# Performance work log

Hardware: AMD Instinct MI355X
Metric: run time of the kernel (lower is better)

Reference implementation:

```python
import jax, jax.numpy as jnp
import numpy as np

IGNORE_LABEL = 7
BETA = 1.0 / 9.0  # smooth-L1 beta from fastrcnn_loss


def setup_inputs() -> dict:
    key = jax.random.key(0)
    k = jax.random.split(key, 12)
    N, C, K, HM, G = 1024, 8, 17, 56, 256
    class_logits = jax.random.normal(k[0], (N, C), dtype=jnp.float32)
    box_regression = jax.random.normal(k[1], (N, C * 4), dtype=jnp.float32)
    regression_targets = jax.random.normal(k[2], (N, 4), dtype=jnp.float32) * 0.2
    # valid xyxy proposals in a ~1000px tile, widths/heights in [8, 64]
    x1 = jax.random.uniform(k[3], (N,)) * 900.0
    y1 = jax.random.uniform(k[4], (N,)) * 900.0
    w = 8.0 + jax.random.uniform(k[5], (N,)) * 56.0
    h = 8.0 + jax.random.uniform(k[6], (N,)) * 56.0
    proposals = jnp.stack([x1, y1, x1 + w, y1 + h], axis=1)
    # ground-truth keypoints: (x, y, visibility)
    kp_xy = jax.random.uniform(k[7], (G, K, 2)) * 1000.0
    kp_vis = (jax.random.uniform(k[8], (G, K, 1)) > 0.3).astype(jnp.float32)
    gt_keypoints = jnp.concatenate([kp_xy, kp_vis], axis=-1)
    keypoint_logits = jax.random.normal(k[9], (N, K, HM, HM), dtype=jnp.float32)
    labels = jax.random.randint(k[10], (N,), 0, C)
    keypoint_matched_idxs = jax.random.randint(k[11], (N,), 0, G)
    return {
        "class_logits": class_logits,
        "box_regression": box_regression,
        "regression_targets": regression_targets,
        "proposals": proposals,
        "gt_keypoints": gt_keypoints,
        "keypoint_logits": keypoint_logits,
        "labels": labels,
        "keypoint_matched_idxs": keypoint_matched_idxs,
    }


def _masked_ce(logits, targets, mask):
    # cross entropy averaged over masked entries (== F.cross_entropy on the subset)
    logp = jax.nn.log_softmax(logits, axis=-1)
    nll = -jnp.take_along_axis(logp, targets[:, None], axis=1)[:, 0]
    cnt = jnp.maximum(jnp.sum(mask.astype(logits.dtype)), 1.0)
    return jnp.sum(jnp.where(mask, nll, 0.0)) / cnt


def reference(class_logits, box_regression, regression_targets, proposals,
              gt_keypoints, keypoint_logits, labels, keypoint_matched_idxs):
    N, C = class_logits.shape
    # ---- fastrcnn_loss ----
    clkeep = labels != IGNORE_LABEL
    classification_loss = _masked_ce(class_logits, labels, clkeep)

    pos = labels > 0  # sampled_pos_inds_subset
    br = box_regression.reshape(N, C, 4)
    sel = jnp.take_along_axis(br, labels[:, None, None], axis=1)[:, 0, :]  # [N,4]
    d = sel - regression_targets
    ad = jnp.abs(d)
    sl1 = jnp.where(ad < BETA, 0.5 * d * d / BETA, ad - 0.5 * BETA)  # smooth_l1, sum
    box_loss = jnp.sum(jnp.where(pos[:, None], sl1, 0.0)) / N

    # ---- keypointrcnn_loss (keypoints_to_heatmap + CE over H*W bins) ----
    Nk, K, H, W = keypoint_logits.shape  # H == W == discretization_size
    kp = gt_keypoints[keypoint_matched_idxs]  # [N,K,3]
    ox, oy = proposals[:, 0:1], proposals[:, 1:2]
    sx = H / (proposals[:, 2:3] - proposals[:, 0:1])
    sy = H / (proposals[:, 3:4] - proposals[:, 1:2])
    kx, ky, vis = kp[..., 0], kp[..., 1], kp[..., 2]
    x = jnp.floor((kx - ox) * sx).astype(jnp.int32)
    y = jnp.floor((ky - oy) * sy).astype(jnp.int32)
    x = jnp.where(kx == proposals[:, 2:3], H - 1, x)
    y = jnp.where(ky == proposals[:, 3:4], H - 1, y)
    valid = (x >= 0) & (y >= 0) & (x < H) & (y < H) & (vis > 0)
    lin = (y * H + x) * valid.astype(jnp.int32)  # invalid entries -> bin 0 (masked out)
    kp_logits = keypoint_logits.reshape(Nk * K, H * W)
    keypoint_loss = _masked_ce(kp_logits, lin.reshape(-1), valid.reshape(-1))

    return jnp.stack([classification_loss, box_loss, keypoint_loss])
```

## Files before the change

### kernel.cpp

```cpp
#include <hip/hip_runtime.h>
#include <math.h>

#define K_KP 17
#define HM 56
#define HW (HM * HM)
#define N_ROWS 1024
#define NK_ROWS (N_ROWS * K_KP)
#define KP_BLOCKS ((NK_ROWS + 3) / 4)
#define C_CLS 8
#define IGNORE_LABEL 7
#define BETA_C (1.0f / 9.0f)

#define WS_FLOATS 515

__global__ __launch_bounds__(256) void roiheads_fused(
    const float* __restrict__ class_logits,
    const float* __restrict__ box_regression,
    const float* __restrict__ regression_targets,
    const float* __restrict__ proposals,
    const float* __restrict__ gt_keypoints,
    const float* __restrict__ keypoint_logits,
    const int*   __restrict__ labels,
    const int*   __restrict__ kmi,
    float* __restrict__ ws)
{
    const int bid = blockIdx.x;
    const int tid = threadIdx.x;

    if (bid < KP_BLOCKS) {
        const int lane = tid & 63;
        const int wid  = tid >> 6;
        const int r = bid * 4 + wid;
        if (r >= NK_ROWS) return;

        const int n = r / K_KP;
        const int k = r - n * K_KP;

        const int g = kmi[n];
        const float* kp = gt_keypoints + ((size_t)g * K_KP + k) * 3;
        const float kx  = kp[0];
        const float ky  = kp[1];
        const float vis = kp[2];
        const float px1 = proposals[n * 4 + 0];
        const float py1 = proposals[n * 4 + 1];
        const float px2 = proposals[n * 4 + 2];
        const float py2 = proposals[n * 4 + 3];
        const float sx = (float)HM / (px2 - px1);
        const float sy = (float)HM / (py2 - py1);
        int xi = (int)floorf((kx - px1) * sx);
        int yi = (int)floorf((ky - py1) * sy);
        if (kx == px2) xi = HM - 1;
        if (ky == py2) yi = HM - 1;
        const bool valid = (xi >= 0) & (yi >= 0) & (xi < HM) & (yi < HM) & (vis > 0.0f);
        if (!valid) return;

        const int lin = yi * HM + xi;
        const float4* rowp = (const float4*)(keypoint_logits + (size_t)r * HW);

        float m = -INFINITY, s = 0.0f;
        #pragma unroll
        for (int it = 0; it < 13; ++it) {
            const int idx = it * 64 + lane;
            if (idx < HW / 4) {
                const float4 v = rowp[idx];
                float vals[4] = {v.x, v.y, v.z, v.w};
                #pragma unroll
                for (int j = 0; j < 4; ++j) {
                    const float x = vals[j];
                    if (x > m) { s = s * expf(m - x) + 1.0f; m = x; }
                    else       { s += expf(x - m); }
                }
            }
        }
        #pragma unroll
        for (int off = 32; off > 0; off >>= 1) {
            const float om = __shfl_down(m, off, 64);
            const float os = __shfl_down(s, off, 64);
            const float nm = fmaxf(m, om);
            s = s * expf(m - nm) + os * expf(om - nm);
            m = nm;
        }
        if (lane == 0) {
            const float xt = keypoint_logits[(size_t)r * HW + lin];
            const float nll = m + logf(s) - xt;
            atomicAdd(&ws[r & 255], nll);
            atomicAdd(&ws[256 + (r & 255)], 1.0f);
        }
    } else {
        const int n = (bid - KP_BLOCKS) * 256 + tid;
        const int label = labels[n];

        const float* cl = class_logits + (size_t)n * C_CLS;
        float m = cl[0];
        #pragma unroll
        for (int j = 1; j < C_CLS; ++j) m = fmaxf(m, cl[j]);
        float s = 0.0f;
        #pragma unroll
        for (int j = 0; j < C_CLS; ++j) s += expf(cl[j] - m);
        const float nll = m + logf(s) - cl[label];
        const float keep = (label != IGNORE_LABEL) ? 1.0f : 0.0f;
        float cls_part = keep * nll;
        float keep_part = keep;

        float box_part = 0.0f;
        if (label > 0) {
            #pragma unroll
            for (int j = 0; j < 4; ++j) {
                const float d = box_regression[(size_t)n * 32 + label * 4 + j]
                              - regression_targets[(size_t)n * 4 + j];
                const float ad = fabsf(d);
                box_part += (ad < BETA_C) ? 0.5f * d * d / BETA_C : ad - 0.5f * BETA_C;
            }
        }

        #pragma unroll
        for (int off = 32; off > 0; off >>= 1) {
            cls_part  += __shfl_down(cls_part,  off, 64);
            keep_part += __shfl_down(keep_part, off, 64);
            box_part  += __shfl_down(box_part,  off, 64);
        }
        if ((tid & 63) == 0) {
            atomicAdd(&ws[512], cls_part);
            atomicAdd(&ws[513], keep_part);
            atomicAdd(&ws[514], box_part);
        }
    }
}

__global__ __launch_bounds__(256) void roiheads_finalize(
    const float* __restrict__ ws, float* __restrict__ out)
{
    __shared__ float sm_s[4];
    __shared__ float sm_c[4];
    const int tid = threadIdx.x;
    float ks = ws[tid];
    float kc = ws[256 + tid];
    #pragma unroll
    for (int off = 32; off > 0; off >>= 1) {
        ks += __shfl_down(ks, off, 64);
        kc += __shfl_down(kc, off, 64);
    }
    const int wid = tid >> 6;
    if ((tid & 63) == 0) { sm_s[wid] = ks; sm_c[wid] = kc; }
    __syncthreads();
    if (tid == 0) {
        const float S  = sm_s[0] + sm_s[1] + sm_s[2] + sm_s[3];
        const float Cn = sm_c[0] + sm_c[1] + sm_c[2] + sm_c[3];
        out[0] = ws[512] / fmaxf(ws[513], 1.0f);
        out[1] = ws[514] / (float)N_ROWS;
        out[2] = S / fmaxf(Cn, 1.0f);
    }
}

extern "C" void kernel_launch(void* const* d_in, const int* in_sizes, int n_in,
                              void* d_out, int out_size, void* d_ws, size_t ws_size,
                              hipStream_t stream) {
    const float* class_logits       = (const float*)d_in[0];
    const float* box_regression     = (const float*)d_in[1];
    const float* regression_targets = (const float*)d_in[2];
    const float* proposals          = (const float*)d_in[3];
    const float* gt_keypoints       = (const float*)d_in[4];
    const float* keypoint_logits    = (const float*)d_in[5];
    const int*   labels             = (const int*)d_in[6];
    const int*   kmi                = (const int*)d_in[7];
    float* ws  = (float*)d_ws;
    float* out = (float*)d_out;

    hipMemsetAsync(ws, 0, WS_FLOATS * sizeof(float), stream);

    const int total_blocks = KP_BLOCKS + (N_ROWS / 256);
    roiheads_fused<<<total_blocks, 256, 0, stream>>>(
        class_logits, box_regression, regression_targets, proposals,
        gt_keypoints, keypoint_logits, labels, kmi, ws);

    roiheads_finalize<<<1, 256, 0, stream>>>(ws, out);
}
```

Measured before the change: 272.5 us.

## Compact valid keypoint rows per block and replace global atomics with slot reduction

Each of 68 blocks now checks validity for 256 keypoint rows at once and appends the valid rows to a shared-memory queue. Its four waves then run the softmax cross-entropy only over the queued rows, which replaces thousands of small blocks that mostly exited early. Per-block partial sums go to fixed workspace slots, and the finalize kernel reduces them. This removes the memset and the global atomics. The tradeoff is less parallelism when many rows are valid, since each wave processes its rows one after another.

```diff
diff --git a/kernel.cpp b/kernel.cpp
--- a/kernel.cpp
+++ b/kernel.cpp
@@ -6,14 +6,14 @@
 #define HW (HM * HM)
 #define N_ROWS 1024
 #define NK_ROWS (N_ROWS * K_KP)
-#define KP_BLOCKS ((NK_ROWS + 3) / 4)
+#define KP_META_BLOCKS (NK_ROWS / 256)
+#define GRID (KP_META_BLOCKS + 1)
 #define C_CLS 8
 #define IGNORE_LABEL 7
 #define BETA_C (1.0f / 9.0f)
 
-#define WS_FLOATS 515
 
-__global__ __launch_bounds__(256) void roiheads_fused(
+__global__ __launch_bounds__(256) void roiheads_main(
     const float* __restrict__ class_logits,
     const float* __restrict__ box_regression,
     const float* __restrict__ regression_targets,
@@ -24,131 +24,154 @@
     const int*   __restrict__ kmi,
     float* __restrict__ ws)
 {
-    const int bid = blockIdx.x;
-    const int tid = threadIdx.x;
+    const int bid  = blockIdx.x;
+    const int tid  = threadIdx.x;
+    const int lane = tid & 63;
+    const int wid  = tid >> 6;
 
-    if (bid < KP_BLOCKS) {
-        const int lane = tid & 63;
-        const int wid  = tid >> 6;
-        const int r = bid * 4 + wid;
-        if (r >= NK_ROWS) return;
+    __shared__ int   q_r[256];
+    __shared__ int   q_lin[256];
+    __shared__ int   q_cnt;
+    __shared__ float w0[4], w1[4], w2[4];
 
+    float p0 = 0.0f, p1 = 0.0f, p2 = 0.0f, p3 = 0.0f, p4 = 0.0f;
+
+    if (bid < KP_META_BLOCKS) {
+        if (tid == 0) q_cnt = 0;
+        __syncthreads();
+
+        const int r = bid * 256 + tid;
         const int n = r / K_KP;
         const int k = r - n * K_KP;
-
         const int g = kmi[n];
         const float* kp = gt_keypoints + ((size_t)g * K_KP + k) * 3;
         const float kx  = kp[0];
         const float ky  = kp[1];
         const float vis = kp[2];
-        const float px1 = proposals[n * 4 + 0];
-        const float py1 = proposals[n * 4 + 1];
-        const float px2 = proposals[n * 4 + 2];
-        const float py2 = proposals[n * 4 + 3];
-        const float sx = (float)HM / (px2 - px1);
-        const float sy = (float)HM / (py2 - py1);
-        int xi = (int)floorf((kx - px1) * sx);
-        int yi = (int)floorf((ky - py1) * sy);
-        if (kx == px2) xi = HM - 1;
-        if (ky == py2) yi = HM - 1;
+        const float4 pr = ((const float4*)proposals)[n];
+        const float sx = (float)HM / (pr.z - pr.x);
+        const float sy = (float)HM / (pr.w - pr.y);
+        int xi = (int)floorf((kx - pr.x) * sx);
+        int yi = (int)floorf((ky - pr.y) * sy);
+        if (kx == pr.z) xi = HM - 1;
+        if (ky == pr.w) yi = HM - 1;
         const bool valid = (xi >= 0) & (yi >= 0) & (xi < HM) & (yi < HM) & (vis > 0.0f);
-        if (!valid) return;
+        if (valid) {
+            const int p = atomicAdd(&q_cnt, 1);
+            q_r[p]   = r;
+            q_lin[p] = yi * HM + xi;
+        }
+        __syncthreads();
+        const int cnt = q_cnt;
 
-        const int lin = yi * HM + xi;
-        const float4* rowp = (const float4*)(keypoint_logits + (size_t)r * HW);
-
-        float m = -INFINITY, s = 0.0f;
+        float my_s = 0.0f, my_c = 0.0f;
+        for (int i = wid; i < cnt; i += 4) {
+            const int rr = q_r[i];
+            const float* row = keypoint_logits + (size_t)rr * HW;
+            const float4* rp = (const float4*)row;
+            float m = -INFINITY, s = 0.0f;
+            #pragma unroll
+            for (int it = 0; it < 13; ++it) {
+                const int idx = it * 64 + lane;
+                if (idx < HW / 4) {
+                    const float4 v = rp[idx];
+                    float vals[4] = {v.x, v.y, v.z, v.w};
+                    #pragma unroll
+                    for (int j = 0; j < 4; ++j) {
+                        const float x = vals[j];
+                        if (x > m) { s = s * expf(m - x) + 1.0f; m = x; }
+                        else       { s += expf(x - m); }
+                    }
+                }
+            }
+            #pragma unroll
+            for (int off = 32; off > 0; off >>= 1) {
+                const float om = __shfl_down(m, off, 64);
+                const float os = __shfl_down(s, off, 64);
+                const float nm = fmaxf(m, om);
+                s = s * expf(m - nm) + os * expf(om - nm);
+                m = nm;
+            }
+            if (lane == 0) {
+                const float xt = row[q_lin[i]];
+                my_s += m + logf(s) - xt;
+                my_c += 1.0f;
+            }
+        }
+        if (lane == 0) { w0[wid] = my_s; w1[wid] = my_c; }
+        __syncthreads();
+        if (tid == 0) {
+            p0 = w0[0] + w0[1] + w0[2] + w0[3];
+            p1 = w1[0] + w1[1] + w1[2] + w1[3];
+        }
+    } else {
+        float cls_part = 0.0f, keep_part = 0.0f, box_part = 0.0f;
         #pragma unroll
-        for (int it = 0; it < 13; ++it) {
-            const int idx = it * 64 + lane;
-            if (idx < HW / 4) {
-                const float4 v = rowp[idx];
-                float vals[4] = {v.x, v.y, v.z, v.w};
+        for (int j = 0; j < 4; ++j) {
+            const int n = j * 256 + tid;
+            const int label = labels[n];
+            const float* cl = class_logits + (size_t)n * C_CLS;
+            float m = cl[0];
+            #pragma unroll
+            for (int c = 1; c < C_CLS; ++c) m = fmaxf(m, cl[c]);
+            float s = 0.0f;
+            #pragma unroll
+            for (int c = 0; c < C_CLS; ++c) s += expf(cl[c] - m);
+            const float nll  = m + logf(s) - cl[label];
+            const float keep = (label != IGNORE_LABEL) ? 1.0f : 0.0f;
+            cls_part  += keep * nll;
+            keep_part += keep;
+            if (label > 0) {
                 #pragma unroll
-                for (int j = 0; j < 4; ++j) {
-                    const float x = vals[j];
-                    if (x > m) { s = s * expf(m - x) + 1.0f; m = x; }
-                    else       { s += expf(x - m); }
+                for (int c = 0; c < 4; ++c) {
+                    const float d = box_regression[(size_t)n * 32 + label * 4 + c]
+                                  - regression_targets[(size_t)n * 4 + c];
+                    const float ad = fabsf(d);
+                    box_part += (ad < BETA_C) ? 0.5f * d * d / BETA_C : ad - 0.5f * BETA_C;
                 }
             }
         }
-        #pragma unroll
-        for (int off = 32; off > 0; off >>= 1) {
-            const float om = __shfl_down(m, off, 64);
-            const float os = __shfl_down(s, off, 64);
-            const float nm = fmaxf(m, om);
-            s = s * expf(m - nm) + os * expf(om - nm);
-            m = nm;
-        }
-        if (lane == 0) {
-            const float xt = keypoint_logits[(size_t)r * HW + lin];
-            const float nll = m + logf(s) - xt;
-            atomicAdd(&ws[r & 255], nll);
-            atomicAdd(&ws[256 + (r & 255)], 1.0f);
-        }
-    } else {
-        const int n = (bid - KP_BLOCKS) * 256 + tid;
-        const int label = labels[n];
-
-        const float* cl = class_logits + (size_t)n * C_CLS;
-        float m = cl[0];
-        #pragma unroll
-        for (int j = 1; j < C_CLS; ++j) m = fmaxf(m, cl[j]);
-        float s = 0.0f;
-        #pragma unroll
-        for (int j = 0; j < C_CLS; ++j) s += expf(cl[j] - m);
-        const float nll = m + logf(s) - cl[label];
-        const float keep = (label != IGNORE_LABEL) ? 1.0f : 0.0f;
-        float cls_part = keep * nll;
-        float keep_part = keep;
-
-        float box_part = 0.0f;
-        if (label > 0) {
-            #pragma unroll
-            for (int j = 0; j < 4; ++j) {
-                const float d = box_regression[(size_t)n * 32 + label * 4 + j]
-                              - regression_targets[(size_t)n * 4 + j];
-                const float ad = fabsf(d);
-                box_part += (ad < BETA_C) ? 0.5f * d * d / BETA_C : ad - 0.5f * BETA_C;
-            }
-        }
-
         #pragma unroll
         for (int off = 32; off > 0; off >>= 1) {
             cls_part  += __shfl_down(cls_part,  off, 64);
             keep_part += __shfl_down(keep_part, off, 64);
             box_part  += __shfl_down(box_part,  off, 64);
         }
-        if ((tid & 63) == 0) {
-            atomicAdd(&ws[512], cls_part);
-            atomicAdd(&ws[513], keep_part);
-            atomicAdd(&ws[514], box_part);
+        if (lane == 0) { w0[wid] = cls_part; w1[wid] = keep_part; w2[wid] = box_part; }
+        __syncthreads();
+        if (tid == 0) {
+            p2 = w0[0] + w0[1] + w0[2] + w0[3];
+            p3 = w1[0] + w1[1] + w1[2] + w1[3];
+            p4 = w2[0] + w2[1] + w2[2] + w2[3];
         }
+    }
+
+    if (tid == 0) {
+        float* slot = ws + (size_t)bid * 5;
+        slot[0] = p0; slot[1] = p1; slot[2] = p2; slot[3] = p3; slot[4] = p4;
     }
 }
 
-__global__ __launch_bounds__(256) void roiheads_finalize(
+__global__ __launch_bounds__(128) void roiheads_finalize(
     const float* __restrict__ ws, float* __restrict__ out)
 {
-    __shared__ float sm_s[4];
-    __shared__ float sm_c[4];
+    __shared__ float acc[5];
     const int tid = threadIdx.x;
-    float ks = ws[tid];
-    float kc = ws[256 + tid];
+    if (tid < 5) acc[tid] = 0.0f;
+    __syncthreads();
+    float v[5] = {0.0f, 0.0f, 0.0f, 0.0f, 0.0f};
+    if (tid < GRID) {
+        const float* slot = ws + (size_t)tid * 5;
+        #pragma unroll
+        for (int j = 0; j < 5; ++j) v[j] = slot[j];
+    }
     #pragma unroll
-    for (int off = 32; off > 0; off >>= 1) {
-        ks += __shfl_down(ks, off, 64);
-        kc += __shfl_down(kc, off, 64);
-    }
-    const int wid = tid >> 6;
-    if ((tid & 63) == 0) { sm_s[wid] = ks; sm_c[wid] = kc; }
+    for (int j = 0; j < 5; ++j) atomicAdd(&acc[j], v[j]);
     __syncthreads();
     if (tid == 0) {
-        const float S  = sm_s[0] + sm_s[1] + sm_s[2] + sm_s[3];
-        const float Cn = sm_c[0] + sm_c[1] + sm_c[2] + sm_c[3];
-        out[0] = ws[512] / fmaxf(ws[513], 1.0f);
-        out[1] = ws[514] / (float)N_ROWS;
-        out[2] = S / fmaxf(Cn, 1.0f);
+        out[0] = acc[2] / fmaxf(acc[3], 1.0f);
+        out[1] = acc[4] / (float)N_ROWS;
+        out[2] = acc[0] / fmaxf(acc[1], 1.0f);
     }
 }
 
@@ -166,12 +189,9 @@
     float* ws  = (float*)d_ws;
     float* out = (float*)d_out;
 
-    hipMemsetAsync(ws, 0, WS_FLOATS * sizeof(float), stream);
-
-    const int total_blocks = KP_BLOCKS + (N_ROWS / 256);
-    roiheads_fused<<<total_blocks, 256, 0, stream>>>(
+    roiheads_main<<<GRID, 256, 0, stream>>>(
         class_logits, box_regression, regression_targets, proposals,
         gt_keypoints, keypoint_logits, labels, kmi, ws);
 
-    roiheads_finalize<<<1, 256, 0, stream>>>(ws, out);
+    roiheads_finalize<<<1, 128, 0, stream>>>(ws, out);
 }
```

After: 275.5 us. No clear change (+1.1%).
